# Kernel tuning notes

Measured on AMD Instinct MI355X. Metric: run time of the kernel, lower is better.

Reference implementation:

```python
import jax, jax.numpy as jnp
import numpy as np

NL, H, N, CIN, COUT, B, L = 4, 256, 64, 64, 8, 8, 1024
LN_EPS = 1e-5


def layernorm(x, w, b):
    m = x.mean(-1, keepdims=True)
    v = ((x - m) ** 2).mean(-1, keepdims=True)
    return (x - m) / jnp.sqrt(v + LN_EPS) * w + b


def s4d(u, A, C, D, log_step):
    # u: [B, H, L] real; A: [N] complex; C: [H, N] complex
    Lq = u.shape[-1]
    step = jnp.exp(log_step)                       # [H]
    dA = step[:, None] * A[None, :]                # [H, N] complex
    C_bar = C * (jnp.exp(dA) - 1.0) / A[None, :]   # [H, N]
    l = jnp.arange(Lq, dtype=jnp.float32)
    P = jnp.exp(l[:, None, None] * dA[None])       # [L, H, N] complex (dominant intermediate)
    K = jnp.einsum('hn,lhn->hl', C_bar, P)         # [H, L] complex
    kf = jnp.fft.rfft(K.real, n=2 * Lq) + 1j * jnp.fft.rfft(K.imag, n=2 * Lq)  # [H, L+1]
    uf = jnp.fft.rfft(u, n=2 * Lq)                 # [B, H, L+1]
    y = jnp.fft.irfft(kf * uf, n=2 * Lq)[..., :Lq]  # [B, H, L] real
    return y + u * D[:, None]


def forward(stimulus_seq, initial_state, A_re, A_im, C_re, C_im, D, log_step,
            ln1_w, ln1_b, ln2_w, ln2_b, W1, b1, W2, b2,
            Win, b_in, Wst, b_st, Wout, b_out):
    # stimulus_seq: [B, CIN, L] -> [B, L, CIN]
    x = stimulus_seq.transpose(0, 2, 1) @ Win.T + b_in            # [B, L, H]
    x = x + (initial_state @ Wst.T + b_st)[:, None, :]            # fusion_mode='add'
    for i in range(NL):
        xn = layernorm(x, ln1_w[i], ln1_b[i])
        A = A_re[i] + 1j * A_im[i]
        C = C_re[i] + 1j * C_im[i]
        y = s4d(xn.transpose(0, 2, 1), A, C, D[i], log_step[i])
        x = x + y.transpose(0, 2, 1)
        xn = layernorm(x, ln2_w[i], ln2_b[i])
        h = jax.nn.gelu(xn @ W1[i].T + b1[i], approximate=False)  # torch GELU = exact erf
        x = x + h @ W2[i].T + b2[i]
    out = x @ Wout.T + b_out                                      # [B, L, COUT]
    # use_voltage_filter=False: split + concat is identity on channel axis
    return out.transpose(0, 2, 1)                                 # [B, COUT, L]


def setup_inputs() -> dict:
    key = jax.random.key(0)
    ks = iter(jax.random.split(key, 24))
    def u(shape, fan_in):
        lim = 1.0 / np.sqrt(fan_in)
        return jax.random.uniform(next(ks), shape, minval=-lim, maxval=lim, dtype=jnp.float32)
    inp = {
        'stimulus_seq': jax.random.normal(next(ks), (B, CIN, L), dtype=jnp.float32),
        'initial_state': jax.random.normal(next(ks), (B, COUT), dtype=jnp.float32),
        'A_re': -0.5 * jnp.ones((NL, N), dtype=jnp.float32),
        'A_im': jnp.tile(jnp.arange(N, dtype=jnp.float32) * np.float32(np.pi), (NL, 1)),
        'C_re': jax.random.normal(next(ks), (NL, H, N), dtype=jnp.float32),
        'C_im': jax.random.normal(next(ks), (NL, H, N), dtype=jnp.float32),
        'D': jax.random.normal(next(ks), (NL, H), dtype=jnp.float32),
        'log_step': jax.random.uniform(next(ks), (NL, H), dtype=jnp.float32) * np.float32(np.log(0.1) - np.log(1e-4)) + np.float32(np.log(1e-4)),
        'ln1_w': jnp.ones((NL, H), dtype=jnp.float32),
        'ln1_b': jnp.zeros((NL, H), dtype=jnp.float32),
        'ln2_w': jnp.ones((NL, H), dtype=jnp.float32),
        'ln2_b': jnp.zeros((NL, H), dtype=jnp.float32),
        'W1': u((NL, 2 * H, H), H), 'b1': u((NL, 2 * H), H),
        'W2': u((NL, H, 2 * H), 2 * H), 'b2': u((NL, H), 2 * H),
        'Win': u((H, CIN), CIN), 'b_in': u((H,), CIN),
        'Wst': u((H, COUT), COUT), 'b_st': u((H,), COUT),
        'Wout': u((COUT, H), H), 'b_out': u((COUT,), H),
    }
    return inp


def reference(stimulus_seq, initial_state, A_re, A_im, C_re, C_im, D, log_step,
              ln1_w, ln1_b, ln2_w, ln2_b, W1, b1, W2, b2,
              Win, b_in, Wst, b_st, Wout, b_out):
    return forward(stimulus_seq, initial_state, A_re, A_im, C_re, C_im, D, log_step,
                   ln1_w, ln1_b, ln2_w, ln2_b, W1, b1, W2, b2,
                   Win, b_in, Wst, b_st, Wout, b_out)
```

## Files before the change

kernel.cpp:

```cpp
#include <hip/hip_runtime.h>
#include <math.h>

#define NL   4
#define H    256
#define NST  64
#define CIN  64
#define COUT 8
#define BB   8
#define LL   1024
#define NFFT 2048

typedef __attribute__((ext_vector_type(8))) short bf16x8;
typedef __attribute__((ext_vector_type(4))) short short4v;
typedef __attribute__((ext_vector_type(4))) int   int4v;
typedef __attribute__((ext_vector_type(4))) float f32x4;

__device__ __forceinline__ short f2bf(float f) {
  union { float f; unsigned u; } v; v.f = f;
  unsigned r = (v.u + 0x7fffu + ((v.u >> 16) & 1u)) >> 16;
  return (short)r;
}
__device__ __forceinline__ int IDX2(int a) { return a + (a >> 4); }
#define FBUF 2176

__device__ __forceinline__ float2 cadd(float2 a, float2 b) { return make_float2(a.x + b.x, a.y + b.y); }
__device__ __forceinline__ float2 csub(float2 a, float2 b) { return make_float2(a.x - b.x, a.y - b.y); }

template <int SGN, bool PADDED>
__device__ __forceinline__ void fft2048(float2* b0, float2* b1,
                                        const float2* __restrict__ tw, int tid) {
  const float RH = 0.70710678118654752f;
  float2 *s = b0, *d = b1;
#pragma unroll
  for (int st = 0; st < 3; ++st) {
    const int m = 1 << (3 * st);
    __syncthreads();
    const int k  = tid & (m - 1);
    const int jm = tid - k;
    float2 a0 = s[IDX2(tid)];
    float2 a1 = s[IDX2(tid + 256)];
    float2 a2 = s[IDX2(tid + 512)];
    float2 a3 = s[IDX2(tid + 768)];
    float2 a4, a5, a6, a7;
    if (PADDED && st == 0) {
      a4 = make_float2(0.f, 0.f); a5 = a4; a6 = a4; a7 = a4;
    } else {
      a4 = s[IDX2(tid + 1024)];
      a5 = s[IDX2(tid + 1280)];
      a6 = s[IDX2(tid + 1536)];
      a7 = s[IDX2(tid + 1792)];
    }
    float2 s0 = cadd(a0, a4), s1 = csub(a0, a4), s2 = cadd(a2, a6), s3 = csub(a2, a6);
    float2 mi = (SGN < 0) ? make_float2(s3.y, -s3.x) : make_float2(-s3.y, s3.x);
    float2 E0 = cadd(s0, s2), E1 = cadd(s1, mi), E2 = csub(s0, s2), E3 = csub(s1, mi);
    float2 t0 = cadd(a1, a5), t1 = csub(a1, a5), t2 = cadd(a3, a7), t3 = csub(a3, a7);
    float2 mj = (SGN < 0) ? make_float2(t3.y, -t3.x) : make_float2(-t3.y, t3.x);
    float2 O0 = cadd(t0, t2), O1 = cadd(t1, mj), O2 = csub(t0, t2), O3 = csub(t1, mj);
    float2 W0 = O0;
    float2 W1 = (SGN < 0) ? make_float2((O1.x + O1.y) * RH, (O1.y - O1.x) * RH)
                          : make_float2((O1.x - O1.y) * RH, (O1.x + O1.y) * RH);
    float2 W2 = (SGN < 0) ? make_float2(O2.y, -O2.x) : make_float2(-O2.y, O2.x);
    float2 W3 = (SGN < 0) ? make_float2((O3.y - O3.x) * RH, -(O3.x + O3.y) * RH)
                          : make_float2(-(O3.x + O3.y) * RH, (O3.x - O3.y) * RH);
    float2 A[8];
    A[0] = cadd(E0, W0); A[4] = csub(E0, W0);
    A[1] = cadd(E1, W1); A[5] = csub(E1, W1);
    A[2] = cadd(E2, W2); A[6] = csub(E2, W2);
    A[3] = cadd(E3, W3); A[7] = csub(E3, W3);
    const int base = 8 * jm + k;
    d[IDX2(base)] = A[0];
#pragma unroll
    for (int dd = 1; dd < 8; ++dd) {
      float2 w = tw[dd * jm];
      float wi = (SGN < 0) ? w.y : -w.y;
      float2 v = A[dd];
      d[IDX2(base + dd * m)] = make_float2(v.x * w.x - v.y * wi, v.x * wi + v.y * w.x);
    }
    float2* tp = s; s = d; d = tp;
  }
  __syncthreads();
#pragma unroll
  for (int q = 0; q < 2; ++q) {
    const int t = tid + (q << 8);
    float2 x0 = s[IDX2(t)], x1 = s[IDX2(t + 512)];
    float2 x2 = s[IDX2(t + 1024)], x3 = s[IDX2(t + 1536)];
    float2 s0 = cadd(x0, x2), s1 = csub(x0, x2), s2 = cadd(x1, x3), s3 = csub(x1, x3);
    float2 mi = (SGN < 0) ? make_float2(s3.y, -s3.x) : make_float2(-s3.y, s3.x);
    d[IDX2(t)]        = cadd(s0, s2);
    d[IDX2(t + 512)]  = cadd(s1, mi);
    d[IDX2(t + 1024)] = csub(s0, s2);
    d[IDX2(t + 1536)] = csub(s1, mi);
  }
  __syncthreads();
}

__global__ __launch_bounds__(256) void k_setup(
    const float* __restrict__ W1, const float* __restrict__ W2, const float* __restrict__ Win,
    const float* __restrict__ init, const float* __restrict__ Wst,
    const float* __restrict__ bst, const float* __restrict__ bin,
    short* __restrict__ W1s, short* __restrict__ W2s, float* __restrict__ WinT,
    float* __restrict__ sp, float2* __restrict__ tw) {
  int idx = blockIdx.x * 256 + threadIdx.x;
  if (idx < 2048) {
    float s, c;
    sincosf(3.14159265358979323846f * (float)idx / 1024.0f, &s, &c);
    tw[idx] = make_float2(c, -s);
  }
  if (idx < 65536) {
    int i = idx >> 14, c = idx & 16383;
    int cblk = c >> 11, s = (c >> 8) & 7, n = (c >> 6) & 3, lane = c & 63;
    int cl = lane & 15, rg = lane >> 4;
    int col = cblk * 64 + n * 16 + cl;
    const float* srcp = W1 + ((size_t)(i * 512 + col)) * 256 + s * 32 + rg * 8;
    short* dstp = W1s + ((size_t)idx) * 8;
#pragma unroll
    for (int j = 0; j < 8; ++j) dstp[j] = f2bf(srcp[j]);
  } else if (idx < 131072) {
    int t = idx - 65536;
    int i = t >> 14, c = t & 16383;
    int cblk = c >> 11, s = (c >> 7) & 15, n = (c >> 6) & 1, lane = c & 63;
    int cl = lane & 15, rg = lane >> 4;
    int col = cblk * 32 + n * 16 + cl;
    const float* srcp = W2 + ((size_t)(i * 256 + col)) * 512 + s * 32 + rg * 8;
    short* dstp = W2s + ((size_t)t) * 8;
#pragma unroll
    for (int j = 0; j < 8; ++j) dstp[j] = f2bf(srcp[j]);
  }
  if (idx < 256 * 64) {
    int hh = idx / 64, c = idx % 64;
    WinT[c * 256 + hh] = Win[idx];
  }
  if (idx < BB * H) {
    int b = idx >> 8, h = idx & 255;
    float acc = bin[h] + bst[h];
#pragma unroll
    for (int c = 0; c < COUT; ++c) acc += init[b * COUT + c] * Wst[h * COUT + c];
    sp[idx] = acc;
  }
}

__global__ __launch_bounds__(256) void k_in_ln1(
    const float* __restrict__ stim, const float* __restrict__ WinT,
    const float* __restrict__ sp, const float* __restrict__ lw, const float* __restrict__ lb,
    float* __restrict__ x, float* __restrict__ xnT) {
  int blk = blockIdx.x;
  int b_ = blk >> 6, l0 = (blk & 63) << 4;
  int tid = threadIdx.x, wv = tid >> 6, lane = tid & 63;
  __shared__ float sc[16][CIN];
  __shared__ float T[16][256];
#pragma unroll
  for (int it = 0; it < 4; ++it) {
    int idx = tid + (it << 8);
    int r = idx & 15, c = idx >> 4;
    sc[r][c] = stim[(b_ * CIN + c) * LL + l0 + r];
  }
  __syncthreads();
  float4 sp4 = *(const float4*)&sp[b_ * H + lane * 4];
  float4 acc[4] = {sp4, sp4, sp4, sp4};
  for (int c = 0; c < CIN; ++c) {
    float4 wv4 = *(const float4*)&WinT[c * H + lane * 4];
#pragma unroll
    for (int rr = 0; rr < 4; ++rr) {
      float s = sc[wv * 4 + rr][c];
      acc[rr].x += s * wv4.x; acc[rr].y += s * wv4.y;
      acc[rr].z += s * wv4.z; acc[rr].w += s * wv4.w;
    }
  }
  float4 w4 = *(const float4*)&lw[lane * 4];
  float4 c4 = *(const float4*)&lb[lane * 4];
#pragma unroll
  for (int rr = 0; rr < 4; ++rr) {
    int lr = wv * 4 + rr;
    float4 v = acc[rr];
    *(float4*)&x[(((size_t)(b_ << 10) + l0 + lr)) * H + lane * 4] = v;
    float s = v.x + v.y + v.z + v.w;
#pragma unroll
    for (int o = 32; o > 0; o >>= 1) s += __shfl_xor(s, o, 64);
    float m = s * (1.0f / H);
    float dx = v.x - m, dy = v.y - m, dz = v.z - m, dw = v.w - m;
    float q = dx * dx + dy * dy + dz * dz + dw * dw;
#pragma unroll
    for (int o = 32; o > 0; o >>= 1) q += __shfl_xor(q, o, 64);
    float rs = rsqrtf(q * (1.0f / H) + 1e-5f);
    float4 o4;
    o4.x = dx * rs * w4.x + c4.x; o4.y = dy * rs * w4.y + c4.y;
    o4.z = dz * rs * w4.z + c4.z; o4.w = dw * rs * w4.w + c4.w;
    *(float4*)&T[lr][lane * 4] = o4;
  }
  __syncthreads();
  float tmp[16];
#pragma unroll
  for (int l = 0; l < 16; ++l) tmp[l] = T[l][tid];
  float* dst = xnT + ((size_t)(b_ * H + tid)) * LL + l0;
#pragma unroll
  for (int l = 0; l < 16; l += 4) {
    float4 v = {tmp[l], tmp[l + 1], tmp[l + 2], tmp[l + 3]};
    *(float4*)&dst[l] = v;
  }
}

__global__ __launch_bounds__(256) void k_kernelfft(
    const float* __restrict__ A_re, const float* __restrict__ A_im,
    const float* __restrict__ C_re, const float* __restrict__ C_im,
    const float* __restrict__ log_step, const float2* __restrict__ tw,
    float2* __restrict__ kf) {
  int blk = blockIdx.x;
  int i = blk >> 8;
  int tid = threadIdx.x;
  __shared__ float2 cb[NST], Mv[NST];
  __shared__ float2 bufA[FBUF], bufB[FBUF];
  float2* T1 = bufB;
  float2* T2 = bufB + 1024;
  float step = expf(log_step[blk]);
  int n = tid & 63, g = tid >> 6;
  float Ar = A_re[i * NST + n], Ai = A_im[i * NST + n];
  float dr = step * Ar, di = step * Ai;
  float er = expf(dr);
  float sn, cs; sincosf(di, &sn, &cs);
  float Er = er * cs, Ei = er * sn;
  if (g == 0) {
    float nr = Er - 1.0f, ni = Ei;
    float dnm = Ar * Ar + Ai * Ai;
    float qr = (nr * Ar + ni * Ai) / dnm;
    float qi = (ni * Ar - nr * Ai) / dnm;
    float Cr = C_re[(size_t)blk * NST + n], Ci = C_im[(size_t)blk * NST + n];
    cb[n] = make_float2(Cr * qr - Ci * qi, Cr * qi + Ci * qr);
    float pr = 1.f, pi = 0.f;
    T1[n * 16] = make_float2(1.f, 0.f);
    for (int a = 1; a < 16; ++a) {
      float t2 = pr * Er - pi * Ei; pi = pr * Ei + pi * Er; pr = t2;
      T1[n * 16 + a] = make_float2(pr, pi);
    }
  } else if (g == 1) {
    float xr = Er, xi = Ei;
#pragma unroll
    for (int j = 0; j < 4; ++j) { float t2 = xr * xr - xi * xi; xi = 2.f * xr * xi; xr = t2; }
    float pr = 1.f, pi = 0.f;
    T2[n * 16] = make_float2(1.f, 0.f);
    for (int a = 1; a < 16; ++a) {
      float t2 = pr * xr - pi * xi; pi = pr * xi + pi * xr; pr = t2;
      T2[n * 16 + a] = make_float2(pr, pi);
    }
    float mr2 = pr * xr - pi * xi, mi2 = pr * xi + pi * xr;
    Mv[n] = make_float2(mr2, mi2);
  }
  __syncthreads();
  float kr[4] = {0.f, 0.f, 0.f, 0.f}, ki[4] = {0.f, 0.f, 0.f, 0.f};
  const int a_lo = tid & 15, a_hi = tid >> 4;
  for (int nn = 0; nn < NST; ++nn) {
    float2 t1 = T1[nn * 16 + a_lo];
    float2 t2v = T2[nn * 16 + a_hi];
    float pr = t1.x * t2v.x - t1.y * t2v.y;
    float pi = t1.x * t2v.y + t1.y * t2v.x;
    float2 c = cb[nn], m = Mv[nn];
#pragma unroll
    for (int q = 0; q < 4; ++q) {
      kr[q] += c.x * pr - c.y * pi;
      ki[q] += c.x * pi + c.y * pr;
      float t2 = pr * m.x - pi * m.y;
      pi = pr * m.y + pi * m.x;
      pr = t2;
    }
  }
  __syncthreads();
#pragma unroll
  for (int q = 0; q < 4; ++q) {
    int l = tid + (q << 8);
    bufA[IDX2(l)] = make_float2(kr[q], ki[q]);
  }
  fft2048<-1, true>(bufA, bufB, tw, tid);
  float2* kfh = kf + (size_t)blk * 1025;
#pragma unroll
  for (int q = 0; q < 4; ++q) {
    int k = tid + (q << 8);
    kfh[k] = bufA[IDX2(k)];
  }
  if (tid == 0) kfh[1024] = bufA[IDX2(1024)];
}

__global__ __launch_bounds__(256) void k_conv(
    const float* __restrict__ xnT, const float2* __restrict__ kf,
    const float* __restrict__ D, const float2* __restrict__ tw, float* __restrict__ yT) {
  int blk = blockIdx.x;
  int b_ = blk >> 7, hp = blk & 127;
  int h0 = hp * 2, h1 = h0 + 1;
  int r0 = b_ * H + h0;
  int tid = threadIdx.x;
  __shared__ float2 bufA[FBUF], bufB[FBUF];
  float u0[4], u1[4];
  const float* x0 = xnT + (size_t)r0 * LL;
  const float* x1 = x0 + LL;
#pragma unroll
  for (int q = 0; q < 4; ++q) {
    int l = tid + (q << 8);
    float v0 = x0[l], v1 = x1[l];
    u0[q] = v0; u1[q] = v1;
    bufA[IDX2(l)] = make_float2(v0, v1);
  }
  fft2048<-1, true>(bufA, bufB, tw, tid);
  const float2* kf0 = kf + (size_t)h0 * 1025;
  const float2* kf1 = kf + (size_t)h1 * 1025;
#pragma unroll
  for (int q = 0; q < 4; ++q) {
    int k = tid + (q << 8);
    if (k == 0) {
      float2 k0 = kf0[0], k1 = kf1[0];
      float2 F0 = bufA[IDX2(0)], Fn = bufA[IDX2(1024)];
      bufB[IDX2(0)]    = make_float2(F0.x * k0.x, F0.y * k1.x);
      float2 k0n = kf0[1024], k1n = kf1[1024];
      bufB[IDX2(1024)] = make_float2(Fn.x * k0n.x, Fn.y * k1n.x);
    } else {
      float2 F = bufA[IDX2(k)], G = bufA[IDX2(2048 - k)];
      float u0r = 0.5f * (F.x + G.x), u0i = 0.5f * (F.y - G.y);
      float dr_ = 0.5f * (F.x - G.x), di_ = 0.5f * (F.y + G.y);
      float u1r = di_, u1i = -dr_;
      float2 k0 = kf0[k], k1 = kf1[k];
      float z0r = u0r * k0.x - u0i * k0.y, z0i = u0r * k0.y + u0i * k0.x;
      float z1r = u1r * k1.x - u1i * k1.y, z1i = u1r * k1.y + u1i * k1.x;
      bufB[IDX2(k)]        = make_float2(z0r - z1i, z0i + z1r);
      bufB[IDX2(2048 - k)] = make_float2(z0r + z1i, z1r - z0i);
    }
  }
  fft2048<1, false>(bufB, bufA, tw, tid);
  float Dh0 = D[h0], Dh1 = D[h1];
  float* y0 = yT + (size_t)r0 * LL;
  float* y1 = y0 + LL;
#pragma unroll
  for (int q = 0; q < 4; ++q) {
    int l = tid + (q << 8);
    float2 z = bufB[IDX2(l)];
    y0[l] = z.x * (1.0f / NFFT) + Dh0 * u0[q];
    y1[l] = z.y * (1.0f / NFFT) + Dh1 * u1[q];
  }
}

#define TXS 260
template <bool LAST>
__global__ __launch_bounds__(512) void k_mlp(
    const short* __restrict__ W1p, const float* __restrict__ b1p,
    const short* __restrict__ W2p, const float* __restrict__ b2p,
    float* __restrict__ x, const float* __restrict__ yT,
    const float* __restrict__ ln2w, const float* __restrict__ ln2b,
    const float* __restrict__ ln1w, const float* __restrict__ ln1b,
    float* __restrict__ xnT,
    const float* __restrict__ Wout, const float* __restrict__ bout,
    float* __restrict__ out) {
  const int m0 = blockIdx.x * 32;
  const int b_ = m0 >> 10, l0 = m0 & 1023;
  const int tid = threadIdx.x;
  const int lane = tid & 63, wid = tid >> 6;
  const int rg = lane >> 4, cl = lane & 15;
  __shared__ __attribute__((aligned(16))) char smem[52224];
  short* A1  = (short*)smem;
  short* A2  = (short*)(smem + 16896);
  float* red = (float*)(smem + 50176);
  float* Txn = (float*)smem;
  float* wlds = (float*)(smem + 33280);

  float v[2][2][4];
  float wl2[2], bl2[2];
#pragma unroll
  for (int n = 0; n < 2; ++n) {
    int col = wid * 32 + n * 16 + cl;
    wl2[n] = ln2w[col]; bl2[n] = ln2b[col];
  }
  float sum[2][4], sq[2][4];
#pragma unroll
  for (int m = 0; m < 2; ++m)
#pragma unroll
    for (int r = 0; r < 4; ++r) { sum[m][r] = 0.f; sq[m][r] = 0.f; }
#pragma unroll
  for (int m = 0; m < 2; ++m)
#pragma unroll
    for (int n = 0; n < 2; ++n) {
      int col = wid * 32 + n * 16 + cl;
      float4 y4 = *(const float4*)&yT[((size_t)(b_ * H + col)) * LL + l0 + m * 16 + rg * 4];
      float yv[4] = {y4.x, y4.y, y4.z, y4.w};
#pragma unroll
      for (int r = 0; r < 4; ++r) {
        int row = m * 16 + rg * 4 + r;
        float val = x[(size_t)(m0 + row) * H + col] + yv[r];
        v[m][n][r] = val;
        sum[m][r] += val; sq[m][r] += val * val;
      }
    }
#pragma unroll
  for (int m = 0; m < 2; ++m)
#pragma unroll
    for (int r = 0; r < 4; ++r) {
#pragma unroll
      for (int o = 1; o < 16; o <<= 1) {
        sum[m][r] += __shfl_xor(sum[m][r], o, 64);
        sq[m][r]  += __shfl_xor(sq[m][r], o, 64);
      }
    }
  if (cl == 0) {
#pragma unroll
    for (int m = 0; m < 2; ++m)
#pragma unroll
      for (int r = 0; r < 4; ++r) {
        int row = m * 16 + rg * 4 + r;
        red[(wid * 32 + row) * 2]     = sum[m][r];
        red[(wid * 32 + row) * 2 + 1] = sq[m][r];
      }
  }
  __syncthreads();
#pragma unroll
  for (int m = 0; m < 2; ++m)
#pragma unroll
    for (int r = 0; r < 4; ++r) {
      int row = m * 16 + rg * 4 + r;
      float S = 0.f, Q = 0.f;
#pragma unroll
      for (int w = 0; w < 8; ++w) { S += red[(w * 32 + row) * 2]; Q += red[(w * 32 + row) * 2 + 1]; }
      float mean = S * (1.0f / H);
      float var = Q * (1.0f / H) - mean * mean;
      float rs = rsqrtf(var + 1e-5f);
#pragma unroll
      for (int n = 0; n < 2; ++n) {
        int col = wid * 32 + n * 16 + cl;
        A1[row * 264 + col] = f2bf((v[m][n][r] - mean) * rs * wl2[n] + bl2[n]);
      }
    }
  __syncthreads();

  f32x4 acc1[2][4];
#pragma unroll
  for (int m = 0; m < 2; ++m)
#pragma unroll
    for (int n = 0; n < 4; ++n) acc1[m][n] = (f32x4){0.f, 0.f, 0.f, 0.f};
  {
    const short* w1base = W1p + (size_t)wid * 16384 + lane * 8;
#pragma unroll
    for (int s = 0; s < 8; ++s) {
      const int kk = s * 32;
      bf16x8 af[2], bfv[4];
#pragma unroll
      for (int n = 0; n < 4; ++n)
        bfv[n] = *(const bf16x8*)(w1base + (s * 4 + n) * 512);
#pragma unroll
      for (int m = 0; m < 2; ++m)
        af[m] = *(const bf16x8*)&A1[(m * 16 + cl) * 264 + kk + rg * 8];
#pragma unroll
      for (int m = 0; m < 2; ++m)
#pragma unroll
        for (int n = 0; n < 4; ++n)
          acc1[m][n] = __builtin_amdgcn_mfma_f32_16x16x32_bf16(af[m], bfv[n], acc1[m][n], 0, 0, 0);
    }
  }
#pragma unroll
  for (int m = 0; m < 2; ++m)
#pragma unroll
    for (int n = 0; n < 4; ++n) {
      int col = wid * 64 + n * 16 + cl;
      float bb = b1p[col];
#pragma unroll
      for (int r = 0; r < 4; ++r) {
        int row = m * 16 + rg * 4 + r;
        float g = acc1[m][n][r] + bb;
        g = 0.5f * g * (1.0f + erff(g * 0.70710678118654752f));
        A2[row * 520 + col] = f2bf(g);
      }
    }
  __syncthreads();

  f32x4 acc2[2][2];
#pragma unroll
  for (int m = 0; m < 2; ++m)
#pragma unroll
    for (int n = 0; n < 2; ++n) acc2[m][n] = (f32x4){0.f, 0.f, 0.f, 0.f};
  {
    const short* w2base = W2p + (size_t)wid * 16384 + lane * 8;
#pragma unroll
    for (int s = 0; s < 16; ++s) {
      const int kk = s * 32;
      bf16x8 af[2], bfv[2];
#pragma unroll
      for (int n = 0; n < 2; ++n)
        bfv[n] = *(const bf16x8*)(w2base + (s * 2 + n) * 512);
#pragma unroll
      for (int m = 0; m < 2; ++m)
        af[m] = *(const bf16x8*)&A2[(m * 16 + cl) * 520 + kk + rg * 8];
#pragma unroll
      for (int m = 0; m < 2; ++m)
#pragma unroll
        for (int n = 0; n < 2; ++n)
          acc2[m][n] = __builtin_amdgcn_mfma_f32_16x16x32_bf16(af[m], bfv[n], acc2[m][n], 0, 0, 0);
    }
  }

  float bv[2], wl1[2], bl1[2];
#pragma unroll
  for (int n = 0; n < 2; ++n) {
    int col = wid * 32 + n * 16 + cl;
    bv[n] = b2p[col];
    if (!LAST) { wl1[n] = ln1w[col]; bl1[n] = ln1b[col]; }
  }
#pragma unroll
  for (int m = 0; m < 2; ++m)
#pragma unroll
    for (int r = 0; r < 4; ++r) { sum[m][r] = 0.f; sq[m][r] = 0.f; }
#pragma unroll
  for (int m = 0; m < 2; ++m)
#pragma unroll
    for (int n = 0; n < 2; ++n) {
#pragma unroll
      for (int r = 0; r < 4; ++r) {
        float vf = acc2[m][n][r] + bv[n] + v[m][n][r];
        acc2[m][n][r] = vf;
        sum[m][r] += vf; sq[m][r] += vf * vf;
      }
    }

  if (LAST) {
    __syncthreads();
#pragma unroll
    for (int m = 0; m < 2; ++m)
#pragma unroll
      for (int n = 0; n < 2; ++n) {
        int col = wid * 32 + n * 16 + cl;
#pragma unroll
        for (int r = 0; r < 4; ++r) {
          int row = m * 16 + rg * 4 + r;
          Txn[row * TXS + col] = acc2[m][n][r];
        }
      }
#pragma unroll
    for (int it = 0; it < 4; ++it) {
      int idx = tid + (it << 9);
      wlds[(idx >> 8) * 258 + (idx & 255)] = Wout[idx];
    }
    __syncthreads();
    if (tid < 256) {
      int row = tid >> 3, co = tid & 7;
      float p = bout[co];
      const float* tr = Txn + row * TXS;
      const float* wr = wlds + co * 258;
#pragma unroll 4
      for (int c = 0; c < H; ++c) p += tr[c] * wr[c];
      out[((b_ * COUT + co) << 10) + l0 + row] = p;
    }
  } else {
#pragma unroll
    for (int m = 0; m < 2; ++m)
#pragma unroll
      for (int r = 0; r < 4; ++r) {
#pragma unroll
        for (int o = 1; o < 16; o <<= 1) {
          sum[m][r] += __shfl_xor(sum[m][r], o, 64);
          sq[m][r]  += __shfl_xor(sq[m][r], o, 64);
        }
      }
    if (cl == 0) {
#pragma unroll
      for (int m = 0; m < 2; ++m)
#pragma unroll
        for (int r = 0; r < 4; ++r) {
          int row = m * 16 + rg * 4 + r;
          red[(wid * 32 + row) * 2]     = sum[m][r];
          red[(wid * 32 + row) * 2 + 1] = sq[m][r];
        }
    }
    __syncthreads();
#pragma unroll
    for (int m = 0; m < 2; ++m) {
#pragma unroll
      for (int r = 0; r < 4; ++r) {
        int row = m * 16 + rg * 4 + r;
        float S = 0.f, Q = 0.f;
#pragma unroll
        for (int w = 0; w < 8; ++w) { S += red[(w * 32 + row) * 2]; Q += red[(w * 32 + row) * 2 + 1]; }
        float mean = S * (1.0f / H);
        float var = Q * (1.0f / H) - mean * mean;
        float rs = rsqrtf(var + 1e-5f);
#pragma unroll
        for (int n = 0; n < 2; ++n) {
          int col = wid * 32 + n * 16 + cl;
          float vf = acc2[m][n][r];
          x[(size_t)(m0 + row) * H + col] = vf;
          Txn[row * TXS + col] = (vf - mean) * rs * wl1[n] + bl1[n];
        }
      }
    }
    __syncthreads();
    int h = tid & 255, seg = (tid >> 8) * 16;
    float tmp[16];
#pragma unroll
    for (int l = 0; l < 16; ++l) tmp[l] = Txn[(seg + l) * TXS + h];
    float* dst = xnT + ((size_t)(b_ * H + h)) * LL + l0 + seg;
#pragma unroll
    for (int l = 0; l < 16; l += 4) {
      float4 v4 = {tmp[l], tmp[l + 1], tmp[l + 2], tmp[l + 3]};
      *(float4*)&dst[l] = v4;
    }
  }
}

extern "C" void kernel_launch(void* const* d_in, const int* in_sizes, int n_in,
                              void* d_out, int out_size, void* d_ws, size_t ws_size,
                              hipStream_t stream) {
  const float* stim  = (const float*)d_in[0];
  const float* init  = (const float*)d_in[1];
  const float* A_re  = (const float*)d_in[2];
  const float* A_im  = (const float*)d_in[3];
  const float* C_re  = (const float*)d_in[4];
  const float* C_im  = (const float*)d_in[5];
  const float* Dp    = (const float*)d_in[6];
  const float* lstep = (const float*)d_in[7];
  const float* ln1w  = (const float*)d_in[8];
  const float* ln1b  = (const float*)d_in[9];
  const float* ln2w  = (const float*)d_in[10];
  const float* ln2b  = (const float*)d_in[11];
  const float* W1    = (const float*)d_in[12];
  const float* b1    = (const float*)d_in[13];
  const float* W2    = (const float*)d_in[14];
  const float* b2    = (const float*)d_in[15];
  const float* Win   = (const float*)d_in[16];
  const float* bin   = (const float*)d_in[17];
  const float* Wst   = (const float*)d_in[18];
  const float* bst   = (const float*)d_in[19];
  const float* Wout  = (const float*)d_in[20];
  const float* bout  = (const float*)d_in[21];
  float* out = (float*)d_out;
  float* ws = (float*)d_ws;

  size_t o = 0;
  auto alloc = [&](size_t nfloats) { size_t r = o; o += (nfloats + 63) & ~(size_t)63; return r; };
  float*  x    = ws + alloc((size_t)BB * LL * H);
  float*  xnT  = ws + alloc((size_t)BB * H * LL);
  float*  yT   = ws + alloc((size_t)BB * H * LL);
  float2* kf   = (float2*)(ws + alloc((size_t)NL * H * 1025 * 2));
  short*  W1s  = (short*)(ws + alloc((size_t)NL * 512 * 256 / 2));
  short*  W2s  = (short*)(ws + alloc((size_t)NL * 256 * 512 / 2));
  float*  WinT = ws + alloc((size_t)64 * 256);
  float*  sp   = ws + alloc((size_t)BB * H);
  float2* tw   = (float2*)(ws + alloc((size_t)2048 * 2));
  (void)ws_size; (void)in_sizes; (void)n_in; (void)out_size;

  k_setup<<<512, 256, 0, stream>>>(W1, W2, Win, init, Wst, bst, bin,
                                   W1s, W2s, WinT, sp, tw);
  k_kernelfft<<<NL * H, 256, 0, stream>>>(A_re, A_im, C_re, C_im, lstep, tw, kf);
  k_in_ln1<<<BB * 64, 256, 0, stream>>>(stim, WinT, sp, ln1w, ln1b, x, xnT);

  for (int i = 0; i < NL; ++i) {
    k_conv<<<BB * H / 2, 256, 0, stream>>>(xnT, kf + (size_t)i * H * 1025,
                                           Dp + i * H, tw, yT);
    if (i < NL - 1) {
      k_mlp<false><<<256, 512, 0, stream>>>(
          W1s + (size_t)i * 512 * 256, b1 + i * 512,
          W2s + (size_t)i * 256 * 512, b2 + i * H,
          x, yT, ln2w + i * H, ln2b + i * H,
          ln1w + (i + 1) * H, ln1b + (i + 1) * H, xnT,
          nullptr, nullptr, nullptr);
    } else {
      k_mlp<true><<<256, 512, 0, stream>>>(
          W1s + (size_t)i * 512 * 256, b1 + i * 512,
          W2s + (size_t)i * 256 * 512, b2 + i * H,
          x, yT, ln2w + i * H, ln2b + i * H,
          nullptr, nullptr, nullptr,
          Wout, bout, out);
    }
  }
}
```

Baseline: 200.6 us.

## Keep FFT first/last stages in registers and double MLP block threads

The FFT is split into helpers. The first radix-8 stage now reads its input directly from registers instead of LDS. The final radix-4 stage writes straight to registers for the kf and y outputs, which removes LDS round trips and a few barriers in k_kernelfft and k_conv. Separately, k_mlp moves from 512 to 1024 threads per block: each wave now owns 16 columns instead of 32, and the cross-wave reduction layout changes to 16 waves with float4 reads. This spreads per-block work across more waves but cuts per-thread MFMA work and adds barrier cost at a larger block size.

```diff
diff --git a/kernel.cpp b/kernel.cpp
--- a/kernel.cpp
+++ b/kernel.cpp
@@ -26,65 +26,82 @@
 __device__ __forceinline__ float2 cadd(float2 a, float2 b) { return make_float2(a.x + b.x, a.y + b.y); }
 __device__ __forceinline__ float2 csub(float2 a, float2 b) { return make_float2(a.x - b.x, a.y - b.y); }
 
-template <int SGN, bool PADDED>
-__device__ __forceinline__ void fft2048(float2* b0, float2* b1,
-                                        const float2* __restrict__ tw, int tid) {
+template <int SGN>
+__device__ __forceinline__ void bfly8(const float2 a[8], float2 A[8]) {
   const float RH = 0.70710678118654752f;
-  float2 *s = b0, *d = b1;
-#pragma unroll
-  for (int st = 0; st < 3; ++st) {
+  float2 s0 = cadd(a[0], a[4]), s1 = csub(a[0], a[4]);
+  float2 s2 = cadd(a[2], a[6]), s3 = csub(a[2], a[6]);
+  float2 mi = (SGN < 0) ? make_float2(s3.y, -s3.x) : make_float2(-s3.y, s3.x);
+  float2 E0 = cadd(s0, s2), E1 = cadd(s1, mi), E2 = csub(s0, s2), E3 = csub(s1, mi);
+  float2 t0 = cadd(a[1], a[5]), t1 = csub(a[1], a[5]);
+  float2 t2 = cadd(a[3], a[7]), t3 = csub(a[3], a[7]);
+  float2 mj = (SGN < 0) ? make_float2(t3.y, -t3.x) : make_float2(-t3.y, t3.x);
+  float2 O0 = cadd(t0, t2), O1 = cadd(t1, mj), O2 = csub(t0, t2), O3 = csub(t1, mj);
+  float2 W0 = O0;
+  float2 W1 = (SGN < 0) ? make_float2((O1.x + O1.y) * RH, (O1.y - O1.x) * RH)
+                        : make_float2((O1.x - O1.y) * RH, (O1.x + O1.y) * RH);
+  float2 W2 = (SGN < 0) ? make_float2(O2.y, -O2.x) : make_float2(-O2.y, O2.x);
+  float2 W3 = (SGN < 0) ? make_float2((O3.y - O3.x) * RH, -(O3.x + O3.y) * RH)
+                        : make_float2(-(O3.x + O3.y) * RH, (O3.x - O3.y) * RH);
+  A[0] = cadd(E0, W0); A[4] = csub(E0, W0);
+  A[1] = cadd(E1, W1); A[5] = csub(E1, W1);
+  A[2] = cadd(E2, W2); A[6] = csub(E2, W2);
+  A[3] = cadd(E3, W3); A[7] = csub(E3, W3);
+}
+
+template <int SGN>
+__device__ __forceinline__ void fft_stage0_reg(const float2 a[8], float2* d,
+                                               const float2* __restrict__ tw, int tid) {
+  float2 A[8];
+  bfly8<SGN>(a, A);
+  const int base = 8 * tid;
+  d[IDX2(base)] = A[0];
+#pragma unroll
+  for (int dd = 1; dd < 8; ++dd) {
+    float2 w = tw[dd * tid];
+    float wi = (SGN < 0) ? w.y : -w.y;
+    d[IDX2(base + dd)] = make_float2(A[dd].x * w.x - A[dd].y * wi,
+                                     A[dd].x * wi + A[dd].y * w.x);
+  }
+}
+
+template <int SGN>
+__device__ __forceinline__ void fft_mid_stages(float2* bA, float2* bB,
+                                               const float2* __restrict__ tw, int tid) {
+#pragma unroll
+  for (int st = 1; st < 3; ++st) {
+    float2* s = (st == 1) ? bA : bB;
+    float2* d = (st == 1) ? bB : bA;
     const int m = 1 << (3 * st);
     __syncthreads();
     const int k  = tid & (m - 1);
     const int jm = tid - k;
-    float2 a0 = s[IDX2(tid)];
-    float2 a1 = s[IDX2(tid + 256)];
-    float2 a2 = s[IDX2(tid + 512)];
-    float2 a3 = s[IDX2(tid + 768)];
-    float2 a4, a5, a6, a7;
-    if (PADDED && st == 0) {
-      a4 = make_float2(0.f, 0.f); a5 = a4; a6 = a4; a7 = a4;
-    } else {
-      a4 = s[IDX2(tid + 1024)];
-      a5 = s[IDX2(tid + 1280)];
-      a6 = s[IDX2(tid + 1536)];
-      a7 = s[IDX2(tid + 1792)];
-    }
-    float2 s0 = cadd(a0, a4), s1 = csub(a0, a4), s2 = cadd(a2, a6), s3 = csub(a2, a6);
-    float2 mi = (SGN < 0) ? make_float2(s3.y, -s3.x) : make_float2(-s3.y, s3.x);
-    float2 E0 = cadd(s0, s2), E1 = cadd(s1, mi), E2 = csub(s0, s2), E3 = csub(s1, mi);
-    float2 t0 = cadd(a1, a5), t1 = csub(a1, a5), t2 = cadd(a3, a7), t3 = csub(a3, a7);
-    float2 mj = (SGN < 0) ? make_float2(t3.y, -t3.x) : make_float2(-t3.y, t3.x);
-    float2 O0 = cadd(t0, t2), O1 = cadd(t1, mj), O2 = csub(t0, t2), O3 = csub(t1, mj);
-    float2 W0 = O0;
-    float2 W1 = (SGN < 0) ? make_float2((O1.x + O1.y) * RH, (O1.y - O1.x) * RH)
-                          : make_float2((O1.x - O1.y) * RH, (O1.x + O1.y) * RH);
-    float2 W2 = (SGN < 0) ? make_float2(O2.y, -O2.x) : make_float2(-O2.y, O2.x);
-    float2 W3 = (SGN < 0) ? make_float2((O3.y - O3.x) * RH, -(O3.x + O3.y) * RH)
-                          : make_float2(-(O3.x + O3.y) * RH, (O3.x - O3.y) * RH);
-    float2 A[8];
-    A[0] = cadd(E0, W0); A[4] = csub(E0, W0);
-    A[1] = cadd(E1, W1); A[5] = csub(E1, W1);
-    A[2] = cadd(E2, W2); A[6] = csub(E2, W2);
-    A[3] = cadd(E3, W3); A[7] = csub(E3, W3);
+    float2 a[8], A[8];
+#pragma unroll
+    for (int q = 0; q < 8; ++q) a[q] = s[IDX2(tid + 256 * q)];
+    bfly8<SGN>(a, A);
     const int base = 8 * jm + k;
     d[IDX2(base)] = A[0];
 #pragma unroll
     for (int dd = 1; dd < 8; ++dd) {
       float2 w = tw[dd * jm];
       float wi = (SGN < 0) ? w.y : -w.y;
-      float2 v = A[dd];
-      d[IDX2(base + dd * m)] = make_float2(v.x * w.x - v.y * wi, v.x * wi + v.y * w.x);
-    }
-    float2* tp = s; s = d; d = tp;
-  }
+      d[IDX2(base + dd * m)] = make_float2(A[dd].x * w.x - A[dd].y * wi,
+                                           A[dd].x * wi + A[dd].y * w.x);
+    }
+  }
+}
+
+template <int SGN>
+__device__ __forceinline__ void fft_final_r4_lds(const float2* s, float2* d, int tid) {
   __syncthreads();
 #pragma unroll
   for (int q = 0; q < 2; ++q) {
     const int t = tid + (q << 8);
     float2 x0 = s[IDX2(t)], x1 = s[IDX2(t + 512)];
     float2 x2 = s[IDX2(t + 1024)], x3 = s[IDX2(t + 1536)];
-    float2 s0 = cadd(x0, x2), s1 = csub(x0, x2), s2 = cadd(x1, x3), s3 = csub(x1, x3);
+    float2 s0 = cadd(x0, x2), s1 = csub(x0, x2);
+    float2 s2 = cadd(x1, x3), s3 = csub(x1, x3);
     float2 mi = (SGN < 0) ? make_float2(s3.y, -s3.x) : make_float2(-s3.y, s3.x);
     d[IDX2(t)]        = cadd(s0, s2);
     d[IDX2(t + 512)]  = cadd(s1, mi);
@@ -92,6 +109,26 @@
     d[IDX2(t + 1536)] = csub(s1, mi);
   }
   __syncthreads();
+}
+
+template <int SGN>
+__device__ __forceinline__ void fft_final_r4_reg(const float2* s, int tid,
+                                                 float2 out0[4], float2 out1[4]) {
+  __syncthreads();
+#pragma unroll
+  for (int q = 0; q < 2; ++q) {
+    const int t = tid + (q << 8);
+    float2 x0 = s[IDX2(t)], x1 = s[IDX2(t + 512)];
+    float2 x2 = s[IDX2(t + 1024)], x3 = s[IDX2(t + 1536)];
+    float2 s0 = cadd(x0, x2), s1 = csub(x0, x2);
+    float2 s2 = cadd(x1, x3), s3 = csub(x1, x3);
+    float2 mi = (SGN < 0) ? make_float2(s3.y, -s3.x) : make_float2(-s3.y, s3.x);
+    float2* o = q ? out1 : out0;
+    o[0] = cadd(s0, s2);
+    o[1] = cadd(s1, mi);
+    o[2] = csub(s0, s2);
+    o[3] = csub(s1, mi);
+  }
 }
 
 __global__ __launch_bounds__(256) void k_setup(
@@ -262,20 +299,20 @@
       pr = t2;
     }
   }
-  __syncthreads();
-#pragma unroll
-  for (int q = 0; q < 4; ++q) {
-    int l = tid + (q << 8);
-    bufA[IDX2(l)] = make_float2(kr[q], ki[q]);
-  }
-  fft2048<-1, true>(bufA, bufB, tw, tid);
+  float2 a[8];
+#pragma unroll
+  for (int q = 0; q < 4; ++q) a[q] = make_float2(kr[q], ki[q]);
+  a[4] = a[5] = a[6] = a[7] = make_float2(0.f, 0.f);
+  fft_stage0_reg<-1>(a, bufA, tw, tid);
+  fft_mid_stages<-1>(bufA, bufB, tw, tid);
+  float2 F0[4], F1[4];
+  fft_final_r4_reg<-1>(bufA, tid, F0, F1);
   float2* kfh = kf + (size_t)blk * 1025;
-#pragma unroll
-  for (int q = 0; q < 4; ++q) {
-    int k = tid + (q << 8);
-    kfh[k] = bufA[IDX2(k)];
-  }
-  if (tid == 0) kfh[1024] = bufA[IDX2(1024)];
+  kfh[tid]       = F0[0];
+  kfh[tid + 512] = F0[1];
+  kfh[tid + 256] = F1[0];
+  kfh[tid + 768] = F1[1];
+  if (tid == 0) kfh[1024] = F0[2];
 }
 
 __global__ __launch_bounds__(256) void k_conv(
@@ -290,14 +327,18 @@
   float u0[4], u1[4];
   const float* x0 = xnT + (size_t)r0 * LL;
   const float* x1 = x0 + LL;
+  float2 a[8];
 #pragma unroll
   for (int q = 0; q < 4; ++q) {
     int l = tid + (q << 8);
     float v0 = x0[l], v1 = x1[l];
     u0[q] = v0; u1[q] = v1;
-    bufA[IDX2(l)] = make_float2(v0, v1);
-  }
-  fft2048<-1, true>(bufA, bufB, tw, tid);
+    a[q] = make_float2(v0, v1);
+  }
+  a[4] = a[5] = a[6] = a[7] = make_float2(0.f, 0.f);
+  fft_stage0_reg<-1>(a, bufA, tw, tid);
+  fft_mid_stages<-1>(bufA, bufB, tw, tid);
+  fft_final_r4_lds<-1>(bufA, bufB, tid);
   const float2* kf0 = kf + (size_t)h0 * 1025;
   const float2* kf1 = kf + (size_t)h1 * 1025;
 #pragma unroll
@@ -305,38 +346,47 @@
     int k = tid + (q << 8);
     if (k == 0) {
       float2 k0 = kf0[0], k1 = kf1[0];
-      float2 F0 = bufA[IDX2(0)], Fn = bufA[IDX2(1024)];
-      bufB[IDX2(0)]    = make_float2(F0.x * k0.x, F0.y * k1.x);
+      float2 F0 = bufB[IDX2(0)], Fn = bufB[IDX2(1024)];
+      bufA[IDX2(0)]    = make_float2(F0.x * k0.x, F0.y * k1.x);
       float2 k0n = kf0[1024], k1n = kf1[1024];
-      bufB[IDX2(1024)] = make_float2(Fn.x * k0n.x, Fn.y * k1n.x);
+      bufA[IDX2(1024)] = make_float2(Fn.x * k0n.x, Fn.y * k1n.x);
     } else {
-      float2 F = bufA[IDX2(k)], G = bufA[IDX2(2048 - k)];
+      float2 F = bufB[IDX2(k)], G = bufB[IDX2(2048 - k)];
       float u0r = 0.5f * (F.x + G.x), u0i = 0.5f * (F.y - G.y);
       float dr_ = 0.5f * (F.x - G.x), di_ = 0.5f * (F.y + G.y);
       float u1r = di_, u1i = -dr_;
       float2 k0 = kf0[k], k1 = kf1[k];
       float z0r = u0r * k0.x - u0i * k0.y, z0i = u0r * k0.y + u0i * k0.x;
       float z1r = u1r * k1.x - u1i * k1.y, z1i = u1r * k1.y + u1i * k1.x;
-      bufB[IDX2(k)]        = make_float2(z0r - z1i, z0i + z1r);
-      bufB[IDX2(2048 - k)] = make_float2(z0r + z1i, z1r - z0i);
-    }
-  }
-  fft2048<1, false>(bufB, bufA, tw, tid);
+      bufA[IDX2(k)]        = make_float2(z0r - z1i, z0i + z1r);
+      bufA[IDX2(2048 - k)] = make_float2(z0r + z1i, z1r - z0i);
+    }
+  }
+  __syncthreads();
+  float2 g[8];
+#pragma unroll
+  for (int q = 0; q < 8; ++q) g[q] = bufA[IDX2(tid + 256 * q)];
+  fft_stage0_reg<1>(g, bufB, tw, tid);
+  fft_mid_stages<1>(bufB, bufA, tw, tid);
+  float2 z0[4], z1[4];
+  fft_final_r4_reg<1>(bufB, tid, z0, z1);
   float Dh0 = D[h0], Dh1 = D[h1];
   float* y0 = yT + (size_t)r0 * LL;
   float* y1 = y0 + LL;
-#pragma unroll
-  for (int q = 0; q < 4; ++q) {
-    int l = tid + (q << 8);
-    float2 z = bufB[IDX2(l)];
-    y0[l] = z.x * (1.0f / NFFT) + Dh0 * u0[q];
-    y1[l] = z.y * (1.0f / NFFT) + Dh1 * u1[q];
-  }
+  const float s = 1.0f / NFFT;
+  y0[tid]       = z0[0].x * s + Dh0 * u0[0];
+  y0[tid + 256] = z1[0].x * s + Dh0 * u0[1];
+  y0[tid + 512] = z0[1].x * s + Dh0 * u0[2];
+  y0[tid + 768] = z1[1].x * s + Dh0 * u0[3];
+  y1[tid]       = z0[0].y * s + Dh1 * u1[0];
+  y1[tid + 256] = z1[0].y * s + Dh1 * u1[1];
+  y1[tid + 512] = z0[1].y * s + Dh1 * u1[2];
+  y1[tid + 768] = z1[1].y * s + Dh1 * u1[3];
 }
 
 #define TXS 260
 template <bool LAST>
-__global__ __launch_bounds__(512) void k_mlp(
+__global__ __launch_bounds__(1024) void k_mlp(
     const short* __restrict__ W1p, const float* __restrict__ b1p,
     const short* __restrict__ W2p, const float* __restrict__ b2p,
     float* __restrict__ x, const float* __restrict__ yT,
@@ -350,40 +400,30 @@
   const int tid = threadIdx.x;
   const int lane = tid & 63, wid = tid >> 6;
   const int rg = lane >> 4, cl = lane & 15;
-  __shared__ __attribute__((aligned(16))) char smem[52224];
+  __shared__ __attribute__((aligned(16))) char smem[54272];
   short* A1  = (short*)smem;
   short* A2  = (short*)(smem + 16896);
-  float* red = (float*)(smem + 50176);
+  float* redS = (float*)(smem + 50176);
+  float* redQ = (float*)(smem + 52224);
   float* Txn = (float*)smem;
   float* wlds = (float*)(smem + 33280);
 
-  float v[2][2][4];
-  float wl2[2], bl2[2];
-#pragma unroll
-  for (int n = 0; n < 2; ++n) {
-    int col = wid * 32 + n * 16 + cl;
-    wl2[n] = ln2w[col]; bl2[n] = ln2b[col];
-  }
+  const int colA = wid * 16 + cl;
+  float v[2][4];
+  const float wl2 = ln2w[colA], bl2 = ln2b[colA];
   float sum[2][4], sq[2][4];
 #pragma unroll
-  for (int m = 0; m < 2; ++m)
-#pragma unroll
-    for (int r = 0; r < 4; ++r) { sum[m][r] = 0.f; sq[m][r] = 0.f; }
-#pragma unroll
-  for (int m = 0; m < 2; ++m)
-#pragma unroll
-    for (int n = 0; n < 2; ++n) {
-      int col = wid * 32 + n * 16 + cl;
-      float4 y4 = *(const float4*)&yT[((size_t)(b_ * H + col)) * LL + l0 + m * 16 + rg * 4];
-      float yv[4] = {y4.x, y4.y, y4.z, y4.w};
-#pragma unroll
-      for (int r = 0; r < 4; ++r) {
-        int row = m * 16 + rg * 4 + r;
-        float val = x[(size_t)(m0 + row) * H + col] + yv[r];
-        v[m][n][r] = val;
-        sum[m][r] += val; sq[m][r] += val * val;
-      }
-    }
+  for (int m = 0; m < 2; ++m) {
+    float4 y4 = *(const float4*)&yT[((size_t)(b_ * H + colA)) * LL + l0 + m * 16 + rg * 4];
+    float yv[4] = {y4.x, y4.y, y4.z, y4.w};
+#pragma unroll
+    for (int r = 0; r < 4; ++r) {
+      int row = m * 16 + rg * 4 + r;
+      float val = x[(size_t)(m0 + row) * H + colA] + yv[r];
+      v[m][r] = val;
+      sum[m][r] = val; sq[m][r] = val * val;
+    }
+  }
 #pragma unroll
   for (int m = 0; m < 2; ++m)
 #pragma unroll
@@ -400,8 +440,8 @@
 #pragma unroll
       for (int r = 0; r < 4; ++r) {
         int row = m * 16 + rg * 4 + r;
-        red[(wid * 32 + row) * 2]     = sum[m][r];
-        red[(wid * 32 + row) * 2 + 1] = sq[m][r];
+        redS[row * 16 + wid] = sum[m][r];
+        redQ[row * 16 + wid] = sq[m][r];
       }
   }
   __syncthreads();
@@ -412,104 +452,88 @@
       int row = m * 16 + rg * 4 + r;
       float S = 0.f, Q = 0.f;
 #pragma unroll
-      for (int w = 0; w < 8; ++w) { S += red[(w * 32 + row) * 2]; Q += red[(w * 32 + row) * 2 + 1]; }
+      for (int j = 0; j < 4; ++j) {
+        float4 s4 = *(const float4*)&redS[row * 16 + j * 4];
+        float4 q4 = *(const float4*)&redQ[row * 16 + j * 4];
+        S += s4.x + s4.y + s4.z + s4.w;
+        Q += q4.x + q4.y + q4.z + q4.w;
+      }
       float mean = S * (1.0f / H);
       float var = Q * (1.0f / H) - mean * mean;
       float rs = rsqrtf(var + 1e-5f);
-#pragma unroll
-      for (int n = 0; n < 2; ++n) {
-        int col = wid * 32 + n * 16 + cl;
-        A1[row * 264 + col] = f2bf((v[m][n][r] - mean) * rs * wl2[n] + bl2[n]);
-      }
-    }
-  __syncthreads();
-
-  f32x4 acc1[2][4];
+      A1[row * 264 + colA] = f2bf((v[m][r] - mean) * rs * wl2 + bl2);
+    }
+  __syncthreads();
+
+  f32x4 acc1[2][2];
 #pragma unroll
   for (int m = 0; m < 2; ++m)
 #pragma unroll
-    for (int n = 0; n < 4; ++n) acc1[m][n] = (f32x4){0.f, 0.f, 0.f, 0.f};
+    for (int n = 0; n < 2; ++n) acc1[m][n] = (f32x4){0.f, 0.f, 0.f, 0.f};
   {
-    const short* w1base = W1p + (size_t)wid * 16384 + lane * 8;
+    const short* w1base = W1p + ((size_t)(wid >> 1) * 2048 + (wid & 1) * 128 + lane) * 8;
 #pragma unroll
     for (int s = 0; s < 8; ++s) {
       const int kk = s * 32;
-      bf16x8 af[2], bfv[4];
-#pragma unroll
-      for (int n = 0; n < 4; ++n)
-        bfv[n] = *(const bf16x8*)(w1base + (s * 4 + n) * 512);
+      bf16x8 af[2], bfv[2];
+#pragma unroll
+      for (int nn = 0; nn < 2; ++nn)
+        bfv[nn] = *(const bf16x8*)(w1base + (size_t)(s * 256 + nn * 64) * 8);
 #pragma unroll
       for (int m = 0; m < 2; ++m)
         af[m] = *(const bf16x8*)&A1[(m * 16 + cl) * 264 + kk + rg * 8];
 #pragma unroll
       for (int m = 0; m < 2; ++m)
 #pragma unroll
-        for (int n = 0; n < 4; ++n)
-          acc1[m][n] = __builtin_amdgcn_mfma_f32_16x16x32_bf16(af[m], bfv[n], acc1[m][n], 0, 0, 0);
+        for (int nn = 0; nn < 2; ++nn)
+          acc1[m][nn] = __builtin_amdgcn_mfma_f32_16x16x32_bf16(af[m], bfv[nn], acc1[m][nn], 0, 0, 0);
     }
   }
 #pragma unroll
   for (int m = 0; m < 2; ++m)
 #pragma unroll
-    for (int n = 0; n < 4; ++n) {
-      int col = wid * 64 + n * 16 + cl;
+    for (int nn = 0; nn < 2; ++nn) {
+      int col = wid * 32 + nn * 16 + cl;
       float bb = b1p[col];
 #pragma unroll
       for (int r = 0; r < 4; ++r) {
         int row = m * 16 + rg * 4 + r;
-        float g = acc1[m][n][r] + bb;
+        float g = acc1[m][nn][r] + bb;
         g = 0.5f * g * (1.0f + erff(g * 0.70710678118654752f));
         A2[row * 520 + col] = f2bf(g);
       }
     }
   __syncthreads();
 
-  f32x4 acc2[2][2];
-#pragma unroll
-  for (int m = 0; m < 2; ++m)
-#pragma unroll
-    for (int n = 0; n < 2; ++n) acc2[m][n] = (f32x4){0.f, 0.f, 0.f, 0.f};
+  f32x4 acc2[2];
+#pragma unroll
+  for (int m = 0; m < 2; ++m) acc2[m] = (f32x4){0.f, 0.f, 0.f, 0.f};
   {
-    const short* w2base = W2p + (size_t)wid * 16384 + lane * 8;
+    const short* w2base = W2p + ((size_t)(wid >> 1) * 2048 + (wid & 1) * 64 + lane) * 8;
 #pragma unroll
     for (int s = 0; s < 16; ++s) {
       const int kk = s * 32;
-      bf16x8 af[2], bfv[2];
-#pragma unroll
-      for (int n = 0; n < 2; ++n)
-        bfv[n] = *(const bf16x8*)(w2base + (s * 2 + n) * 512);
+      bf16x8 af[2];
+      bf16x8 bfv = *(const bf16x8*)(w2base + (size_t)(s * 128) * 8);
 #pragma unroll
       for (int m = 0; m < 2; ++m)
         af[m] = *(const bf16x8*)&A2[(m * 16 + cl) * 520 + kk + rg * 8];
 #pragma unroll
       for (int m = 0; m < 2; ++m)
-#pragma unroll
-        for (int n = 0; n < 2; ++n)
-          acc2[m][n] = __builtin_amdgcn_mfma_f32_16x16x32_bf16(af[m], bfv[n], acc2[m][n], 0, 0, 0);
-    }
-  }
-
-  float bv[2], wl1[2], bl1[2];
-#pragma unroll
-  for (int n = 0; n < 2; ++n) {
-    int col = wid * 32 + n * 16 + cl;
-    bv[n] = b2p[col];
-    if (!LAST) { wl1[n] = ln1w[col]; bl1[n] = ln1b[col]; }
-  }
+        acc2[m] = __builtin_amdgcn_mfma_f32_16x16x32_bf16(af[m], bfv, acc2[m], 0, 0, 0);
+    }
+  }
+
+  const float bv = b2p[colA];
+  float wl1 = 0.f, bl1 = 0.f;
+  if (!LAST) { wl1 = ln1w[colA]; bl1 = ln1b[colA]; }
 #pragma unroll
   for (int m = 0; m < 2; ++m)
 #pragma unroll
-    for (int r = 0; r < 4; ++r) { sum[m][r] = 0.f; sq[m][r] = 0.f; }
-#pragma unroll
-  for (int m = 0; m < 2; ++m)
-#pragma unroll
-    for (int n = 0; n < 2; ++n) {
-#pragma unroll
-      for (int r = 0; r < 4; ++r) {
-        float vf = acc2[m][n][r] + bv[n] + v[m][n][r];
-        acc2[m][n][r] = vf;
-        sum[m][r] += vf; sq[m][r] += vf * vf;
-      }
+    for (int r = 0; r < 4; ++r) {
+      float vf = acc2[m][r] + bv + v[m][r];
+      acc2[m][r] = vf;
+      sum[m][r] = vf; sq[m][r] = vf * vf;
     }
 
   if (LAST) {
@@ -517,17 +541,13 @@
 #pragma unroll
     for (int m = 0; m < 2; ++m)
 #pragma unroll
-      for (int n = 0; n < 2; ++n) {
-        int col = wid * 32 + n * 16 + cl;
-#pragma unroll
-        for (int r = 0; r < 4; ++r) {
-          int row = m * 16 + rg * 4 + r;
-          Txn[row * TXS + col] = acc2[m][n][r];
-        }
+      for (int r = 0; r < 4; ++r) {
+        int row = m * 16 + rg * 4 + r;
+        Txn[row * TXS + colA] = acc2[m][r];
       }
 #pragma unroll
-    for (int it = 0; it < 4; ++it) {
-      int idx = tid + (it << 9);
+    for (int it = 0; it < 2; ++it) {
+      int idx = tid + (it << 10);
       wlds[(idx >> 8) * 258 + (idx & 255)] = Wout[idx];
     }
     __syncthreads();
@@ -557,8 +577,8 @@
 #pragma unroll
         for (int r = 0; r < 4; ++r) {
           int row = m * 16 + rg * 4 + r;
-          red[(wid * 32 + row) * 2]     = sum[m][r];
-          red[(wid * 32 + row) * 2 + 1] = sq[m][r];
+          redS[row * 16 + wid] = sum[m][r];
+          redQ[row * 16 + wid] = sq[m][r];
         }
     }
     __syncthreads();
@@ -569,27 +589,28 @@
         int row = m * 16 + rg * 4 + r;
         float S = 0.f, Q = 0.f;
 #pragma unroll
-        for (int w = 0; w < 8; ++w) { S += red[(w * 32 + row) * 2]; Q += red[(w * 32 + row) * 2 + 1]; }
+        for (int j = 0; j < 4; ++j) {
+          float4 s4 = *(const float4*)&redS[row * 16 + j * 4];
+          float4 q4 = *(const float4*)&redQ[row * 16 + j * 4];
+          S += s4.x + s4.y + s4.z + s4.w;
+          Q += q4.x + q4.y + q4.z + q4.w;
+        }
         float mean = S * (1.0f / H);
         float var = Q * (1.0f / H) - mean * mean;
         float rs = rsqrtf(var + 1e-5f);
-#pragma unroll
-        for (int n = 0; n < 2; ++n) {
-          int col = wid * 32 + n * 16 + cl;
-          float vf = acc2[m][n][r];
-          x[(size_t)(m0 + row) * H + col] = vf;
-          Txn[row * TXS + col] = (vf - mean) * rs * wl1[n] + bl1[n];
-        }
+        float vf = acc2[m][r];
+        x[(size_t)(m0 + row) * H + colA] = vf;
+        Txn[row * TXS + colA] = (vf - mean) * rs * wl1 + bl1;
       }
     }
     __syncthreads();
-    int h = tid & 255, seg = (tid >> 8) * 16;
-    float tmp[16];
-#pragma unroll
-    for (int l = 0; l < 16; ++l) tmp[l] = Txn[(seg + l) * TXS + h];
+    int h = tid & 255, seg = (tid >> 8) * 8;
+    float tmp[8];
+#pragma unroll
+    for (int l = 0; l < 8; ++l) tmp[l] = Txn[(seg + l) * TXS + h];
     float* dst = xnT + ((size_t)(b_ * H + h)) * LL + l0 + seg;
 #pragma unroll
-    for (int l = 0; l < 16; l += 4) {
+    for (int l = 0; l < 8; l += 4) {
       float4 v4 = {tmp[l], tmp[l + 1], tmp[l + 2], tmp[l + 3]};
       *(float4*)&dst[l] = v4;
     }
@@ -646,14 +667,14 @@
     k_conv<<<BB * H / 2, 256, 0, stream>>>(xnT, kf + (size_t)i * H * 1025,
                                            Dp + i * H, tw, yT);
     if (i < NL - 1) {
-      k_mlp<false><<<256, 512, 0, stream>>>(
+      k_mlp<false><<<256, 1024, 0, stream>>>(
           W1s + (size_t)i * 512 * 256, b1 + i * 512,
           W2s + (size_t)i * 256 * 512, b2 + i * H,
           x, yT, ln2w + i * H, ln2b + i * H,
           ln1w + (i + 1) * H, ln1b + (i + 1) * H, xnT,
           nullptr, nullptr, nullptr);
     } else {
-      k_mlp<true><<<256, 512, 0, stream>>>(
+      k_mlp<true><<<256, 1024, 0, stream>>>(
           W1s + (size_t)i * 512 * 256, b1 + i * 512,
           W2s + (size_t)i * 256 * 512, b2 + i * H,
           x, yT, ln2w + i * H, ln2b + i * H,
```

After: 215.3 us. +7.3%, slower.
